# Kernel tuning notes

Measured on AMD Instinct MI355X. Metric: run time of the kernel, lower is better.

The kernel has to match this reference:

```python
import jax, jax.numpy as jnp
import numpy as np

B, D, L, Q, E, NB, NI = 32, 16, 512, 8, 128, 30, 100000
BN_EPS = 1e-3  # tf.layers.batch_normalization default epsilon
LO, HI = 0.001, 1.0  # histogram_fixed_width value_range
_BN_INV = 1.0 / np.sqrt(1.0 + BN_EPS)  # inference BN with moving_mean=0, moving_var=1


def _bn(x, g, b):
    return g * (x * np.float32(_BN_INV)) + b


def setup_inputs() -> dict:
    key = jax.random.key(0)
    ks = jax.random.split(key, 16)
    dims = [NB, 128, 64, 32, 1]
    inp = {
        "doc": jax.random.randint(ks[0], (B, D, L), 0, NI, dtype=jnp.int32),
        "query": jax.random.randint(ks[1], (B, Q), 0, NI, dtype=jnp.int32),
        "item_embedding": jax.random.normal(ks[2], (NI, E), dtype=jnp.float32),
        "idf_table": jax.random.uniform(ks[3], (NI, 1), dtype=jnp.float32),
        "w_gate": jax.random.normal(ks[4], (Q,), dtype=jnp.float32),
        "g_in": jnp.ones((NB,), jnp.float32),
        "b_in": jnp.zeros((NB,), jnp.float32),
    }
    for i in range(4):
        fan_in, fan_out = dims[i], dims[i + 1]
        kW = jax.random.fold_in(ks[5], i)
        inp[f"W{i}"] = jax.random.normal(kW, (fan_in, fan_out), dtype=jnp.float32) / np.float32(np.sqrt(fan_in))
        inp[f"b{i}"] = jnp.zeros((fan_out,), jnp.float32)
        inp[f"g{i}"] = jnp.ones((fan_out,), jnp.float32)
        inp[f"be{i}"] = jnp.zeros((fan_out,), jnp.float32)
    return inp


def reference(doc, query, item_embedding, idf_table, w_gate, g_in, b_in,
              W0, b0, g0, be0, W1, b1, g1, be1, W2, b2, g2, be2, W3, b3, g3, be3):
    # Embedding lookups
    doc_vec = item_embedding[doc].reshape(B, D * L, E)      # [B, D*L, E]
    q_vec = item_embedding[query]                            # [B, Q, E]
    q_idf = idf_table[query][..., 0]                         # [B, Q]

    # Term gating network: softmax(w * idf) over query terms
    gate = jax.nn.softmax(w_gate * q_idf, axis=-1)           # [B, Q]

    # Cosine similarity of every doc token vs every query term
    d_norm = jnp.sqrt(jnp.sum(doc_vec * doc_vec, axis=-1))   # [B, D*L]
    q_norm = jnp.sqrt(jnp.sum(q_vec * q_vec, axis=-1))       # [B, Q]
    dots = jnp.einsum('bne,bqe->bqn', doc_vec, q_vec)        # [B, Q, D*L]
    sims = dots / (d_norm[:, None, :] * q_norm[:, :, None] + 1e-8)

    # Matching histogram: tf.histogram_fixed_width([0.001, 1], nbins) semantics
    idx = jnp.clip(jnp.floor((sims - LO) / (HI - LO) * NB).astype(jnp.int32), 0, NB - 1)
    rows = B * Q * D
    flat = (jnp.arange(rows, dtype=jnp.int32)[:, None] * NB + idx.reshape(rows, L)).reshape(-1)
    hist = jax.ops.segment_sum(jnp.ones((rows * L,), jnp.float32), flat,
                               num_segments=rows * NB).reshape(B, Q, D, NB)

    # DeepNet: BN -> [dense -> BN -> tanh] x 4 (dropout off at inference)
    x = _bn(hist, g_in, b_in)
    for W, b, g, be in ((W0, b0, g0, be0), (W1, b1, g1, be1),
                        (W2, b2, g2, be2), (W3, b3, g3, be3)):
        x = jnp.tanh(_bn(x @ W + b, g, be))
    query_out = x[..., 0]                                    # [B, Q, D]

    # Score aggregation over query terms
    return jnp.sum(query_out * gate[:, :, None], axis=1)     # [B, D]
```

## Files before the change

kernel.cpp:

```cpp
#include <hip/hip_runtime.h>
#include <math.h>


#define BN_INV 0.99950037468777346f

__device__ __forceinline__ float shflx(float v, int m) {
    return __shfl_xor(v, m, 64);
}

__device__ __forceinline__ int sel8i(int v0, int v1, int v2, int v3,
                                     int v4, int v5, int v6, int v7, int i) {
    int a0 = (i & 1) ? v1 : v0;
    int a1 = (i & 1) ? v3 : v2;
    int a2 = (i & 1) ? v5 : v4;
    int a3 = (i & 1) ? v7 : v6;
    int b0 = (i & 2) ? a1 : a0;
    int b1 = (i & 2) ? a3 : a2;
    return (i & 4) ? b1 : b0;
}

__device__ __forceinline__ float sel8f(float v0, float v1, float v2, float v3,
                                       float v4, float v5, float v6, float v7, int i) {
    float a0 = (i & 1) ? v1 : v0;
    float a1 = (i & 1) ? v3 : v2;
    float a2 = (i & 1) ? v5 : v4;
    float a3 = (i & 1) ? v7 : v6;
    float b0 = (i & 2) ? a1 : a0;
    float b1 = (i & 2) ? a3 : a2;
    return (i & 4) ? b1 : b0;
}

__device__ __forceinline__ float tanh_fast(float x) {
    float y = fminf(fmaxf(x, -9.0f), 9.0f);
    float t = exp2f(y * 2.8853901817f);
    return (t - 1.0f) * __builtin_amdgcn_rcpf(t + 1.0f);
}

__device__ __forceinline__ float4 ld4(const float* base, int elem_off) {
    return *(const float4*)(base + elem_off);
}

#define PIN4(V) asm volatile("" : "+v"((V).x), "+v"((V).y), "+v"((V).z), "+v"((V).w))

template <bool PARTIAL>
__global__ __launch_bounds__(512, 8)
void drmm_hist(const int* __restrict__ doc,
               const int* __restrict__ query,
               const float* __restrict__ emb,
               float* __restrict__ hist_out)
{
    __shared__ float histw[8][8][32];
    __shared__ float qn_s[8];
    __shared__ float4 qlds[8][32];

    const int tid  = threadIdx.x;
    const int bid  = blockIdx.x;
    const int b    = bid >> 7;
    const int wid  = tid >> 6;
    const int lane = tid & 63;
    const int j    = tid & 7;

    const int gtok = bid * 64 + (tid >> 3);
    const int idx  = doc[gtok];

    for (int i = tid; i < 8 * 8 * 32; i += 512) ((float*)histw)[i] = 0.0f;

    const int* qrow = query + b * 8;
    const int qi0 = __builtin_amdgcn_readfirstlane(qrow[0]);
    const int qi1 = __builtin_amdgcn_readfirstlane(qrow[1]);
    const int qi2 = __builtin_amdgcn_readfirstlane(qrow[2]);
    const int qi3 = __builtin_amdgcn_readfirstlane(qrow[3]);
    const int qi4 = __builtin_amdgcn_readfirstlane(qrow[4]);
    const int qi5 = __builtin_amdgcn_readfirstlane(qrow[5]);
    const int qi6 = __builtin_amdgcn_readfirstlane(qrow[6]);
    const int qi7 = __builtin_amdgcn_readfirstlane(qrow[7]);

    if (tid < 256) {
        int q = tid >> 5;
        int c = tid & 31;
        int qis = sel8i(qi0, qi1, qi2, qi3, qi4, qi5, qi6, qi7, q);
        qlds[q][c] = *((const float4*)(emb + (size_t)qis * 128) + c);
    }
    __syncthreads();

    if (wid == 0) {
        int q = lane >> 3, jj = lane & 7;
        float s = 0.f;
#pragma unroll
        for (int c = 0; c < 4; ++c) {
            float4 x = qlds[q][jj * 4 + c];
            s = fmaf(x.x, x.x, s); s = fmaf(x.y, x.y, s);
            s = fmaf(x.z, x.z, s); s = fmaf(x.w, x.w, s);
        }
        s += shflx(s, 1); s += shflx(s, 2); s += shflx(s, 4);
        if (jj == 0) qn_s[q] = sqrtf(s);
    }

    const float* rbase = emb + (size_t)idx * 128;
    const int eo = j * 4;

    float4 A0 = ld4(rbase, eo);
    float4 A1 = ld4(rbase, eo + 32);
    float4 A2 = ld4(rbase, eo + 64);
    float4 A3 = ld4(rbase, eo + 96);

    float dd = 0.f;
    float dq0 = 0.f, dq1 = 0.f, dq2 = 0.f, dq3 = 0.f;
    float dq4 = 0.f, dq5 = 0.f, dq6 = 0.f, dq7 = 0.f;

#define KSTEP(V, K) {                                                       \
        const int S = (K) * 8 + j;                                          \
        float4 v  = (V);                                                    \
        float4 a0 = qlds[0][S], a1 = qlds[1][S];                            \
        float4 a2 = qlds[2][S], a3 = qlds[3][S];                            \
        float4 a4 = qlds[4][S], a5 = qlds[5][S];                            \
        float4 a6 = qlds[6][S], a7 = qlds[7][S];                            \
        dd = fmaf(v.x, v.x, dd); dd = fmaf(v.y, v.y, dd);                   \
        dd = fmaf(v.z, v.z, dd); dd = fmaf(v.w, v.w, dd);                   \
        dq0 = fmaf(v.x, a0.x, dq0); dq0 = fmaf(v.y, a0.y, dq0);             \
        dq0 = fmaf(v.z, a0.z, dq0); dq0 = fmaf(v.w, a0.w, dq0);             \
        dq1 = fmaf(v.x, a1.x, dq1); dq1 = fmaf(v.y, a1.y, dq1);             \
        dq1 = fmaf(v.z, a1.z, dq1); dq1 = fmaf(v.w, a1.w, dq1);             \
        dq2 = fmaf(v.x, a2.x, dq2); dq2 = fmaf(v.y, a2.y, dq2);             \
        dq2 = fmaf(v.z, a2.z, dq2); dq2 = fmaf(v.w, a2.w, dq2);             \
        dq3 = fmaf(v.x, a3.x, dq3); dq3 = fmaf(v.y, a3.y, dq3);             \
        dq3 = fmaf(v.z, a3.z, dq3); dq3 = fmaf(v.w, a3.w, dq3);             \
        dq4 = fmaf(v.x, a4.x, dq4); dq4 = fmaf(v.y, a4.y, dq4);             \
        dq4 = fmaf(v.z, a4.z, dq4); dq4 = fmaf(v.w, a4.w, dq4);             \
        dq5 = fmaf(v.x, a5.x, dq5); dq5 = fmaf(v.y, a5.y, dq5);             \
        dq5 = fmaf(v.z, a5.z, dq5); dq5 = fmaf(v.w, a5.w, dq5);             \
        dq6 = fmaf(v.x, a6.x, dq6); dq6 = fmaf(v.y, a6.y, dq6);             \
        dq6 = fmaf(v.z, a6.z, dq6); dq6 = fmaf(v.w, a6.w, dq6);             \
        dq7 = fmaf(v.x, a7.x, dq7); dq7 = fmaf(v.y, a7.y, dq7);             \
        dq7 = fmaf(v.z, a7.z, dq7); dq7 = fmaf(v.w, a7.w, dq7);             \
    }

    PIN4(A0); KSTEP(A0, 0)
    PIN4(A1); KSTEP(A1, 1)
    PIN4(A2); KSTEP(A2, 2)
    PIN4(A3); KSTEP(A3, 3)
#undef KSTEP

#pragma unroll
    for (int off = 1; off <= 4; off <<= 1) {
        dd  += shflx(dd, off);
        dq0 += shflx(dq0, off); dq1 += shflx(dq1, off);
        dq2 += shflx(dq2, off); dq3 += shflx(dq3, off);
        dq4 += shflx(dq4, off); dq5 += shflx(dq5, off);
        dq6 += shflx(dq6, off); dq7 += shflx(dq7, off);
    }

    __syncthreads();

    {
        float dqj = sel8f(dq0, dq1, dq2, dq3, dq4, dq5, dq6, dq7, j);
        float sim = dqj / (sqrtf(dd) * qn_s[j] + 1e-8f);
        float u = (sim - 0.001f) / 0.999f * 30.0f;
        int bin = (int)floorf(u);
        bin = bin < 0 ? 0 : (bin > 29 ? 29 : bin);
        atomicAdd(&histw[wid][j][bin], 1.0f);
    }
    __syncthreads();

    if (tid < 240) {
        int q = tid / 30, k = tid - q * 30;
        float s = ((histw[0][q][k] + histw[1][q][k])
                 + (histw[2][q][k] + histw[3][q][k]))
                + ((histw[4][q][k] + histw[5][q][k])
                 + (histw[6][q][k] + histw[7][q][k]));
        if (PARTIAL) {
            hist_out[(size_t)bid * 240 + tid] = s;
        } else {
            atomicAdd(&hist_out[(bid >> 3) * 240 + tid], s);
        }
    }
}

template <bool PARTIAL>
__global__ __launch_bounds__(512, 3)
void drmm_mlp(const float* __restrict__ hist_g,
              const int* __restrict__ query,
              const float* __restrict__ idf,
              const float* __restrict__ w_gate,
              const float* __restrict__ g_in, const float* __restrict__ b_in,
              const float* __restrict__ W0, const float* __restrict__ b0,
              const float* __restrict__ g0, const float* __restrict__ be0,
              const float* __restrict__ W1, const float* __restrict__ b1,
              const float* __restrict__ g1, const float* __restrict__ be1,
              const float* __restrict__ W2, const float* __restrict__ b2,
              const float* __restrict__ g2, const float* __restrict__ be2,
              const float* __restrict__ W3, const float* __restrict__ b3,
              const float* __restrict__ g3, const float* __restrict__ be3,
              float* __restrict__ out)
{
    __shared__ float W1l[8192];
    __shared__ float xrow[8][30];
    __shared__ float h1s[8][128];
    __shared__ float h2s[8][64];
    __shared__ float h3s[8][32];
    __shared__ float gate_s[8];
    __shared__ float part[8];

    const int tid  = threadIdx.x;
    const int bd   = blockIdx.x;
    const int b    = bd >> 4;
    const int wid  = tid >> 6;
    const int lane = tid & 63;

#pragma unroll
    for (int i = 0; i < 4; ++i)
        ((float4*)W1l)[tid + i * 512] = ((const float4*)W1)[tid + i * 512];

    if (tid >= 504) {
        int q = tid - 504;
        float z = w_gate[q] * idf[query[b * 8 + q]];
        float m = z;
        m = fmaxf(m, shflx(m, 1)); m = fmaxf(m, shflx(m, 2)); m = fmaxf(m, shflx(m, 4));
        float e = expf(z - m);
        float s = e;
        s += shflx(s, 1); s += shflx(s, 2); s += shflx(s, 4);
        gate_s[q] = e / s;
    }

    if (tid < 240) {
        int q = tid / 30, k = tid - q * 30;
        float s;
        if (PARTIAL) {
            const float* hp = hist_g + (size_t)bd * 8 * 240 + tid;
            s = ((hp[0] + hp[240]) + (hp[480] + hp[720]))
              + ((hp[960] + hp[1200]) + (hp[1440] + hp[1680]));
        } else {
            s = hist_g[bd * 240 + tid];
        }
        xrow[q][k] = g_in[k] * (s * BN_INV) + b_in[k];
    }
    __syncthreads();

    {
        float a0 = 0.f, a1 = 0.f;
#pragma unroll
        for (int k = 0; k < 30; ++k) {
            float xk = xrow[wid][k];
            a0 += xk * W0[k * 128 + lane];
            a1 += xk * W0[k * 128 + 64 + lane];
        }
        a0 += b0[lane]; a1 += b0[lane + 64];
        h1s[wid][lane]      = tanh_fast(g0[lane]      * (a0 * BN_INV) + be0[lane]);
        h1s[wid][lane + 64] = tanh_fast(g0[lane + 64] * (a1 * BN_INV) + be0[lane + 64]);
    }
    __syncthreads();

    {
        float a = 0.f;
#pragma unroll 16
        for (int k = 0; k < 128; ++k) a += h1s[wid][k] * W1l[k * 64 + lane];
        a += b1[lane];
        h2s[wid][lane] = tanh_fast(g1[lane] * (a * BN_INV) + be1[lane]);
    }
    __syncthreads();

    if (lane < 32) {
        float a = 0.f;
#pragma unroll 8
        for (int k = 0; k < 64; ++k) a += h2s[wid][k] * W2[k * 32 + lane];
        a += b2[lane];
        h3s[wid][lane] = tanh_fast(g2[lane] * (a * BN_INV) + be2[lane]);
    }

    if (lane == 0) {
        float a = 0.f;
#pragma unroll
        for (int k = 0; k < 32; ++k) a += h3s[wid][k] * W3[k];
        a += b3[0];
        float y = tanh_fast(g3[0] * (a * BN_INV) + be3[0]);
        part[wid] = gate_s[wid] * y;
    }
    __syncthreads();

    if (tid == 0) {
        float s = 0.f;
#pragma unroll
        for (int q = 0; q < 8; ++q) s += part[q];
        out[bd] = s;
    }
}

extern "C" void kernel_launch(void* const* d_in, const int* in_sizes, int n_in,
                              void* d_out, int out_size, void* d_ws, size_t ws_size,
                              hipStream_t stream) {
    (void)in_sizes; (void)n_in; (void)out_size;
    const int*   doc    = (const int*)d_in[0];
    const int*   query  = (const int*)d_in[1];
    const float* emb    = (const float*)d_in[2];
    const float* idf    = (const float*)d_in[3];
    const float* w_gate = (const float*)d_in[4];
    const float* g_in   = (const float*)d_in[5];
    const float* b_in   = (const float*)d_in[6];
    const float* W0  = (const float*)d_in[7];
    const float* b0  = (const float*)d_in[8];
    const float* g0  = (const float*)d_in[9];
    const float* be0 = (const float*)d_in[10];
    const float* W1  = (const float*)d_in[11];
    const float* b1  = (const float*)d_in[12];
    const float* g1  = (const float*)d_in[13];
    const float* be1 = (const float*)d_in[14];
    const float* W2  = (const float*)d_in[15];
    const float* b2  = (const float*)d_in[16];
    const float* g2  = (const float*)d_in[17];
    const float* be2 = (const float*)d_in[18];
    const float* W3  = (const float*)d_in[19];
    const float* b3  = (const float*)d_in[20];
    const float* g3  = (const float*)d_in[21];
    const float* be3 = (const float*)d_in[22];

    float* hist_g = (float*)d_ws;
    const size_t need_partial = (size_t)4096 * 240 * sizeof(float);

    if (ws_size >= need_partial) {
        drmm_hist<true><<<dim3(4096), dim3(512), 0, stream>>>(doc, query, emb, hist_g);
        drmm_mlp<true><<<dim3(512), dim3(512), 0, stream>>>(
            hist_g, query, idf, w_gate, g_in, b_in,
            W0, b0, g0, be0, W1, b1, g1, be1,
            W2, b2, g2, be2, W3, b3, g3, be3, (float*)d_out);
    } else {
        hipMemsetAsync(hist_g, 0, 512 * 240 * sizeof(float), stream);
        drmm_hist<false><<<dim3(4096), dim3(512), 0, stream>>>(doc, query, emb, hist_g);
        drmm_mlp<false><<<dim3(512), dim3(512), 0, stream>>>(
            hist_g, query, idf, w_gate, g_in, b_in,
            W0, b0, g0, be0, W1, b1, g1, be1,
            W2, b2, g2, be2, W3, b3, g3, be3, (float*)d_out);
    }
}
```

Measured before the change: 47.98 us.

## Process four doc tokens per lane group to reuse query LDS loads

Each 8-lane group now handles four doc tokens instead of one, so every block covers 256 tokens and the grid shrinks from 4096 to 1024 blocks. Query vectors read from LDS are reused across four tokens' dot products, and row loads are double-buffered in two register sets to overlap global gathers with FMAs. Per-block setup (query staging, histogram zeroing, partial writes) is amortized over more tokens, and the MLP kernel sums two partials instead of eight. The cost is much higher register pressure (occupancy hint lowered to 4) and fewer blocks to hide gather latency.

```diff
diff --git a/kernel.cpp b/kernel.cpp
--- a/kernel.cpp
+++ b/kernel.cpp
@@ -42,8 +42,28 @@
 
 #define PIN4(V) asm volatile("" : "+v"((V).x), "+v"((V).y), "+v"((V).z), "+v"((V).w))
 
+#define FMA1(v, A, ACC) ACC = fmaf(v.x, (A).x, ACC); ACC = fmaf(v.y, (A).y, ACC); \
+                        ACC = fmaf(v.z, (A).z, ACC); ACC = fmaf(v.w, (A).w, ACC);
+#define TOKSTEP(V, T) { \
+        float4 v = (V); \
+        dd##T = fmaf(v.x, v.x, dd##T); dd##T = fmaf(v.y, v.y, dd##T); \
+        dd##T = fmaf(v.z, v.z, dd##T); dd##T = fmaf(v.w, v.w, dd##T); \
+        FMA1(v, a0, dq0_##T) FMA1(v, a1, dq1_##T) \
+        FMA1(v, a2, dq2_##T) FMA1(v, a3, dq3_##T) \
+        FMA1(v, a4, dq4_##T) FMA1(v, a5, dq5_##T) \
+        FMA1(v, a6, dq6_##T) FMA1(v, a7, dq7_##T) \
+    }
+#define KBLOCK(R0, R1, R2, R3, K) { \
+        const int S = (K) * 8 + j; \
+        float4 a0 = qlds[0][S], a1 = qlds[1][S]; \
+        float4 a2 = qlds[2][S], a3 = qlds[3][S]; \
+        float4 a4 = qlds[4][S], a5 = qlds[5][S]; \
+        float4 a6 = qlds[6][S], a7 = qlds[7][S]; \
+        TOKSTEP(R0, 0) TOKSTEP(R1, 1) TOKSTEP(R2, 2) TOKSTEP(R3, 3) \
+    }
+
 template <bool PARTIAL>
-__global__ __launch_bounds__(512, 8)
+__global__ __launch_bounds__(512, 4)
 void drmm_hist(const int* __restrict__ doc,
                const int* __restrict__ query,
                const float* __restrict__ emb,
@@ -55,13 +75,14 @@
 
     const int tid  = threadIdx.x;
     const int bid  = blockIdx.x;
-    const int b    = bid >> 7;
+    const int b    = bid >> 5;
     const int wid  = tid >> 6;
     const int lane = tid & 63;
-    const int j    = tid & 7;
-
-    const int gtok = bid * 64 + (tid >> 3);
-    const int idx  = doc[gtok];
+    const int g    = lane >> 3;
+    const int j    = lane & 7;
+
+    const int tokbase = bid * 256 + wid * 32 + g * 4;
+    const int4 idxv = *(const int4*)(doc + tokbase);
 
     for (int i = tid; i < 8 * 8 * 32; i += 512) ((float*)histw)[i] = 0.0f;
 
@@ -76,8 +97,7 @@
     const int qi7 = __builtin_amdgcn_readfirstlane(qrow[7]);
 
     if (tid < 256) {
-        int q = tid >> 5;
-        int c = tid & 31;
+        int q = tid >> 5, c = tid & 31;
         int qis = sel8i(qi0, qi1, qi2, qi3, qi4, qi5, qi6, qi7, q);
         qlds[q][c] = *((const float4*)(emb + (size_t)qis * 128) + c);
     }
@@ -96,70 +116,71 @@
         if (jj == 0) qn_s[q] = sqrtf(s);
     }
 
-    const float* rbase = emb + (size_t)idx * 128;
     const int eo = j * 4;
-
-    float4 A0 = ld4(rbase, eo);
-    float4 A1 = ld4(rbase, eo + 32);
-    float4 A2 = ld4(rbase, eo + 64);
-    float4 A3 = ld4(rbase, eo + 96);
-
-    float dd = 0.f;
-    float dq0 = 0.f, dq1 = 0.f, dq2 = 0.f, dq3 = 0.f;
-    float dq4 = 0.f, dq5 = 0.f, dq6 = 0.f, dq7 = 0.f;
-
-#define KSTEP(V, K) {                                                       \
-        const int S = (K) * 8 + j;                                          \
-        float4 v  = (V);                                                    \
-        float4 a0 = qlds[0][S], a1 = qlds[1][S];                            \
-        float4 a2 = qlds[2][S], a3 = qlds[3][S];                            \
-        float4 a4 = qlds[4][S], a5 = qlds[5][S];                            \
-        float4 a6 = qlds[6][S], a7 = qlds[7][S];                            \
-        dd = fmaf(v.x, v.x, dd); dd = fmaf(v.y, v.y, dd);                   \
-        dd = fmaf(v.z, v.z, dd); dd = fmaf(v.w, v.w, dd);                   \
-        dq0 = fmaf(v.x, a0.x, dq0); dq0 = fmaf(v.y, a0.y, dq0);             \
-        dq0 = fmaf(v.z, a0.z, dq0); dq0 = fmaf(v.w, a0.w, dq0);             \
-        dq1 = fmaf(v.x, a1.x, dq1); dq1 = fmaf(v.y, a1.y, dq1);             \
-        dq1 = fmaf(v.z, a1.z, dq1); dq1 = fmaf(v.w, a1.w, dq1);             \
-        dq2 = fmaf(v.x, a2.x, dq2); dq2 = fmaf(v.y, a2.y, dq2);             \
-        dq2 = fmaf(v.z, a2.z, dq2); dq2 = fmaf(v.w, a2.w, dq2);             \
-        dq3 = fmaf(v.x, a3.x, dq3); dq3 = fmaf(v.y, a3.y, dq3);             \
-        dq3 = fmaf(v.z, a3.z, dq3); dq3 = fmaf(v.w, a3.w, dq3);             \
-        dq4 = fmaf(v.x, a4.x, dq4); dq4 = fmaf(v.y, a4.y, dq4);             \
-        dq4 = fmaf(v.z, a4.z, dq4); dq4 = fmaf(v.w, a4.w, dq4);             \
-        dq5 = fmaf(v.x, a5.x, dq5); dq5 = fmaf(v.y, a5.y, dq5);             \
-        dq5 = fmaf(v.z, a5.z, dq5); dq5 = fmaf(v.w, a5.w, dq5);             \
-        dq6 = fmaf(v.x, a6.x, dq6); dq6 = fmaf(v.y, a6.y, dq6);             \
-        dq6 = fmaf(v.z, a6.z, dq6); dq6 = fmaf(v.w, a6.w, dq6);             \
-        dq7 = fmaf(v.x, a7.x, dq7); dq7 = fmaf(v.y, a7.y, dq7);             \
-        dq7 = fmaf(v.z, a7.z, dq7); dq7 = fmaf(v.w, a7.w, dq7);             \
-    }
-
-    PIN4(A0); KSTEP(A0, 0)
-    PIN4(A1); KSTEP(A1, 1)
-    PIN4(A2); KSTEP(A2, 2)
-    PIN4(A3); KSTEP(A3, 3)
-#undef KSTEP
+    const float* rb0 = emb + (size_t)idxv.x * 128;
+    const float* rb1 = emb + (size_t)idxv.y * 128;
+    const float* rb2 = emb + (size_t)idxv.z * 128;
+    const float* rb3 = emb + (size_t)idxv.w * 128;
+
+    float4 RA0 = ld4(rb0, eo),      RA1 = ld4(rb1, eo);
+    float4 RA2 = ld4(rb2, eo),      RA3 = ld4(rb3, eo);
+    float4 RB0 = ld4(rb0, eo + 32), RB1 = ld4(rb1, eo + 32);
+    float4 RB2 = ld4(rb2, eo + 32), RB3 = ld4(rb3, eo + 32);
+
+    float dd0 = 0.f, dd1 = 0.f, dd2 = 0.f, dd3 = 0.f;
+    float dq0_0=0.f, dq1_0=0.f, dq2_0=0.f, dq3_0=0.f, dq4_0=0.f, dq5_0=0.f, dq6_0=0.f, dq7_0=0.f;
+    float dq0_1=0.f, dq1_1=0.f, dq2_1=0.f, dq3_1=0.f, dq4_1=0.f, dq5_1=0.f, dq6_1=0.f, dq7_1=0.f;
+    float dq0_2=0.f, dq1_2=0.f, dq2_2=0.f, dq3_2=0.f, dq4_2=0.f, dq5_2=0.f, dq6_2=0.f, dq7_2=0.f;
+    float dq0_3=0.f, dq1_3=0.f, dq2_3=0.f, dq3_3=0.f, dq4_3=0.f, dq5_3=0.f, dq6_3=0.f, dq7_3=0.f;
+
+    PIN4(RA0); PIN4(RA1); PIN4(RA2); PIN4(RA3);
+    KBLOCK(RA0, RA1, RA2, RA3, 0)
+    RA0 = ld4(rb0, eo + 64); RA1 = ld4(rb1, eo + 64);
+    RA2 = ld4(rb2, eo + 64); RA3 = ld4(rb3, eo + 64);
+    PIN4(RB0); PIN4(RB1); PIN4(RB2); PIN4(RB3);
+    KBLOCK(RB0, RB1, RB2, RB3, 1)
+    RB0 = ld4(rb0, eo + 96); RB1 = ld4(rb1, eo + 96);
+    RB2 = ld4(rb2, eo + 96); RB3 = ld4(rb3, eo + 96);
+    PIN4(RA0); PIN4(RA1); PIN4(RA2); PIN4(RA3);
+    KBLOCK(RA0, RA1, RA2, RA3, 2)
+    PIN4(RB0); PIN4(RB1); PIN4(RB2); PIN4(RB3);
+    KBLOCK(RB0, RB1, RB2, RB3, 3)
 
 #pragma unroll
     for (int off = 1; off <= 4; off <<= 1) {
-        dd  += shflx(dd, off);
-        dq0 += shflx(dq0, off); dq1 += shflx(dq1, off);
-        dq2 += shflx(dq2, off); dq3 += shflx(dq3, off);
-        dq4 += shflx(dq4, off); dq5 += shflx(dq5, off);
-        dq6 += shflx(dq6, off); dq7 += shflx(dq7, off);
-    }
-
-    __syncthreads();
-
-    {
-        float dqj = sel8f(dq0, dq1, dq2, dq3, dq4, dq5, dq6, dq7, j);
-        float sim = dqj / (sqrtf(dd) * qn_s[j] + 1e-8f);
-        float u = (sim - 0.001f) / 0.999f * 30.0f;
-        int bin = (int)floorf(u);
-        bin = bin < 0 ? 0 : (bin > 29 ? 29 : bin);
-        atomicAdd(&histw[wid][j][bin], 1.0f);
-    }
+        dd0 += shflx(dd0, off); dd1 += shflx(dd1, off);
+        dd2 += shflx(dd2, off); dd3 += shflx(dd3, off);
+        dq0_0 += shflx(dq0_0, off); dq1_0 += shflx(dq1_0, off);
+        dq2_0 += shflx(dq2_0, off); dq3_0 += shflx(dq3_0, off);
+        dq4_0 += shflx(dq4_0, off); dq5_0 += shflx(dq5_0, off);
+        dq6_0 += shflx(dq6_0, off); dq7_0 += shflx(dq7_0, off);
+        dq0_1 += shflx(dq0_1, off); dq1_1 += shflx(dq1_1, off);
+        dq2_1 += shflx(dq2_1, off); dq3_1 += shflx(dq3_1, off);
+        dq4_1 += shflx(dq4_1, off); dq5_1 += shflx(dq5_1, off);
+        dq6_1 += shflx(dq6_1, off); dq7_1 += shflx(dq7_1, off);
+        dq0_2 += shflx(dq0_2, off); dq1_2 += shflx(dq1_2, off);
+        dq2_2 += shflx(dq2_2, off); dq3_2 += shflx(dq3_2, off);
+        dq4_2 += shflx(dq4_2, off); dq5_2 += shflx(dq5_2, off);
+        dq6_2 += shflx(dq6_2, off); dq7_2 += shflx(dq7_2, off);
+        dq0_3 += shflx(dq0_3, off); dq1_3 += shflx(dq1_3, off);
+        dq2_3 += shflx(dq2_3, off); dq3_3 += shflx(dq3_3, off);
+        dq4_3 += shflx(dq4_3, off); dq5_3 += shflx(dq5_3, off);
+        dq6_3 += shflx(dq6_3, off); dq7_3 += shflx(dq7_3, off);
+    }
+
+    __syncthreads();
+
+#define DOBIN(T) { \
+        float dqj = sel8f(dq0_##T, dq1_##T, dq2_##T, dq3_##T, \
+                          dq4_##T, dq5_##T, dq6_##T, dq7_##T, j); \
+        float sim = dqj / (sqrtf(dd##T) * qn_s[j] + 1e-8f); \
+        float u = (sim - 0.001f) / 0.999f * 30.0f; \
+        int bin = (int)floorf(u); \
+        bin = bin < 0 ? 0 : (bin > 29 ? 29 : bin); \
+        atomicAdd(&histw[wid][j][bin], 1.0f); \
+    }
+    DOBIN(0) DOBIN(1) DOBIN(2) DOBIN(3)
+#undef DOBIN
     __syncthreads();
 
     if (tid < 240) {
@@ -171,7 +192,7 @@
         if (PARTIAL) {
             hist_out[(size_t)bid * 240 + tid] = s;
         } else {
-            atomicAdd(&hist_out[(bid >> 3) * 240 + tid], s);
+            atomicAdd(&hist_out[(bid >> 1) * 240 + tid], s);
         }
     }
 }
@@ -226,9 +247,8 @@
         int q = tid / 30, k = tid - q * 30;
         float s;
         if (PARTIAL) {
-            const float* hp = hist_g + (size_t)bd * 8 * 240 + tid;
-            s = ((hp[0] + hp[240]) + (hp[480] + hp[720]))
-              + ((hp[960] + hp[1200]) + (hp[1440] + hp[1680]));
+            const float* hp = hist_g + (size_t)bd * 480 + tid;
+            s = hp[0] + hp[240];
         } else {
             s = hist_g[bd * 240 + tid];
         }
@@ -314,17 +334,17 @@
     const float* be3 = (const float*)d_in[22];
 
     float* hist_g = (float*)d_ws;
-    const size_t need_partial = (size_t)4096 * 240 * sizeof(float);
+    const size_t need_partial = (size_t)1024 * 240 * sizeof(float);
 
     if (ws_size >= need_partial) {
-        drmm_hist<true><<<dim3(4096), dim3(512), 0, stream>>>(doc, query, emb, hist_g);
+        drmm_hist<true><<<dim3(1024), dim3(512), 0, stream>>>(doc, query, emb, hist_g);
         drmm_mlp<true><<<dim3(512), dim3(512), 0, stream>>>(
             hist_g, query, idf, w_gate, g_in, b_in,
             W0, b0, g0, be0, W1, b1, g1, be1,
             W2, b2, g2, be2, W3, b3, g3, be3, (float*)d_out);
     } else {
         hipMemsetAsync(hist_g, 0, 512 * 240 * sizeof(float), stream);
-        drmm_hist<false><<<dim3(4096), dim3(512), 0, stream>>>(doc, query, emb, hist_g);
+        drmm_hist<false><<<dim3(1024), dim3(512), 0, stream>>>(doc, query, emb, hist_g);
         drmm_mlp<false><<<dim3(512), dim3(512), 0, stream>>>(
             hist_g, query, idf, w_gate, g_in, b_in,
             W0, b0, g0, be0, W1, b1, g1, be1,
```

Result: no change. 47.11 us (-1.8%).
